# Performance work log

Measured on AMD Instinct MI355X. Metric: run time of the kernel, lower is better.

Reference implementation:

```python
import jax, jax.numpy as jnp
import numpy as np

N, E, T = 32768, 262144, 262144
DN, DE = 128, 128
EPS = 1e-5  # torch LayerNorm default eps


def layer_norm(x, g, b):
    m = jnp.mean(x, axis=-1, keepdims=True)
    v = jnp.mean((x - m) ** 2, axis=-1, keepdims=True)
    return (x - m) * jax.lax.rsqrt(v + EPS) * g + b


def setup_inputs() -> dict:
    key = jax.random.key(0)
    ks = jax.random.split(key, 16)
    node_embedding = jax.random.normal(ks[0], (N, DN), dtype=jnp.float32)
    edge_embedding = jax.random.normal(ks[1], (E, DE), dtype=jnp.float32)
    i = jax.random.randint(ks[2], (E,), 0, N)
    j = jax.random.randint(ks[3], (E,), 0, N)
    index_i = jax.random.randint(ks[4], (T,), 0, N)
    index_j = jax.random.randint(ks[5], (T,), 0, N)
    index_k = jax.random.randint(ks[6], (T,), 0, N)
    index_ji = jax.random.randint(ks[7], (T,), 0, E)
    index_kj = jax.random.randint(ks[8], (T,), 0, E)
    d3 = 3 * DN + 2 * DE
    W2 = jax.random.normal(ks[9], (2 * DE, DN), dtype=jnp.float32) / np.sqrt(DN)
    b2 = jnp.zeros((2 * DE,), dtype=jnp.float32)
    W3 = jax.random.normal(ks[10], (2 * DE, d3), dtype=jnp.float32) / np.sqrt(d3)
    b3 = jnp.zeros((2 * DE,), dtype=jnp.float32)
    g_c2 = jnp.ones((2 * DE,), jnp.float32); be_c2 = jnp.zeros((2 * DE,), jnp.float32)
    g_c3 = jnp.ones((2 * DE,), jnp.float32); be_c3 = jnp.zeros((2 * DE,), jnp.float32)
    g_c2_2 = jnp.ones((DE,), jnp.float32); be_c2_2 = jnp.zeros((DE,), jnp.float32)
    g_c3_2 = jnp.ones((DE,), jnp.float32); be_c3_2 = jnp.zeros((DE,), jnp.float32)
    return dict(node_embedding=node_embedding, edge_embedding=edge_embedding,
                i=i, j=j, index_i=index_i, index_j=index_j, index_k=index_k,
                index_ji=index_ji, index_kj=index_kj,
                W2=W2, b2=b2, W3=W3, b3=b3,
                g_c2=g_c2, be_c2=be_c2, g_c3=g_c3, be_c3=be_c3,
                g_c2_2=g_c2_2, be_c2_2=be_c2_2, g_c3_2=g_c3_2, be_c3_2=be_c3_2)


def reference(node_embedding, edge_embedding, i, j, index_i, index_j, index_k,
              index_ji, index_kj, W2, b2, W3, b3,
              g_c2, be_c2, g_c3, be_c3, g_c2_2, be_c2_2, g_c3_2, be_c3_2):
    num_edges = edge_embedding.shape[0]
    # --- c2 branch: per-edge elementwise product of endpoint node embeddings ---
    c2 = node_embedding[i] * node_embedding[j]                      # [E, Dn]
    c2 = layer_norm(c2 @ W2.T + b2, g_c2, be_c2)                    # [E, 2De]
    c2_filter, c2_core = jnp.split(c2, 2, axis=1)
    c2_emb = layer_norm(jax.nn.sigmoid(c2_filter) * jnp.tanh(c2_core), g_c2_2, be_c2_2)
    # --- c3 branch: triplet gather -> linear -> LN -> gate -> scatter-sum ---
    c3 = jnp.concatenate([node_embedding[index_i], node_embedding[index_j],
                          node_embedding[index_k], edge_embedding[index_ji],
                          edge_embedding[index_kj]], axis=1)        # [T, 3Dn+2De]
    c3 = layer_norm(c3 @ W3.T + b3, g_c3, be_c3)                    # [T, 2De]
    c3_filter, c3_core = jnp.split(c3, 2, axis=1)
    msg = jax.nn.sigmoid(c3_filter) * jnp.tanh(c3_core)             # [T, De]
    c3_emb = jax.ops.segment_sum(msg, index_ji, num_segments=num_edges)  # [E, De]
    c3_emb = layer_norm(c3_emb, g_c3_2, be_c3_2)
    return jnp.tanh(edge_embedding + c2_emb + c3_emb)
```

## Files before the change

### kernel.cpp

```cpp
#include <hip/hip_runtime.h>

typedef _Float16 h16;
typedef _Float16 h16x8 __attribute__((ext_vector_type(8)));
typedef float    f32x4 __attribute__((ext_vector_type(4)));

static constexpr int NN  = 32768;
static constexpr int EE  = 262144;
static constexpr int TT  = 262144;
static constexpr int D   = 128;
static constexpr int K3  = 640;
static constexpr int LDA = 72;
#define EPS 1e-5f

__device__ __forceinline__ float fast_rcp(float x) { return __builtin_amdgcn_rcpf(x); }
__device__ __forceinline__ float fast_tanh(float x) {
    const float e = __expf(2.f * x);
    return 1.f - 2.f * fast_rcp(e + 1.f);
}
__device__ __forceinline__ float fast_sig(float x) {
    return fast_rcp(1.f + __expf(-x));
}

__global__ __launch_bounds__(256) void cvt_f32_f16(
    const float* __restrict__ src, h16* __restrict__ dst, int n8)
{
    const int i = blockIdx.x * 256 + threadIdx.x;
    if (i >= n8) return;
    const float4* s = reinterpret_cast<const float4*>(src);
    const float4 a = s[2 * i], b = s[2 * i + 1];
    h16x8 o;
    o[0] = (h16)a.x; o[1] = (h16)a.y; o[2] = (h16)a.z; o[3] = (h16)a.w;
    o[4] = (h16)b.x; o[5] = (h16)b.y; o[6] = (h16)b.z; o[7] = (h16)b.w;
    *reinterpret_cast<h16x8*>(dst + 8 * i) = o;
}

__global__ __launch_bounds__(256) void cvt_edge_zero(
    const float* __restrict__ src, h16* __restrict__ dst,
    float* __restrict__ zbuf, int n8)
{
    const int i = blockIdx.x * 256 + threadIdx.x;
    if (i >= n8) return;
    const float4* s = reinterpret_cast<const float4*>(src);
    const float4 a = s[2 * i], b = s[2 * i + 1];
    h16x8 o;
    o[0] = (h16)a.x; o[1] = (h16)a.y; o[2] = (h16)a.z; o[3] = (h16)a.w;
    o[4] = (h16)b.x; o[5] = (h16)b.y; o[6] = (h16)b.z; o[7] = (h16)b.w;
    *reinterpret_cast<h16x8*>(dst + 8 * i) = o;
    const float4 z = {0.f, 0.f, 0.f, 0.f};
    float4* zp = reinterpret_cast<float4*>(zbuf);
    zp[2 * i]     = z;
    zp[2 * i + 1] = z;
}

__global__ __launch_bounds__(256) void cvt_w_t(
    const float* __restrict__ src, h16* __restrict__ dst, int K, int n8)
{
    const int t = blockIdx.x * 256 + threadIdx.x;
    if (t >= n8) return;
    const int d   = t * 8;
    const int c   = d >> 14;
    const int rem = d & 16383;
    const int q   = rem >> 11;
    const int n   = (rem >> 3) & 255;
    const int k   = c * 64 + q * 8;
    const float4* s = reinterpret_cast<const float4*>(src + (size_t)n * K + k);
    const float4 a = s[0], b = s[1];
    h16x8 o;
    o[0] = (h16)a.x; o[1] = (h16)a.y; o[2] = (h16)a.z; o[3] = (h16)a.w;
    o[4] = (h16)b.x; o[5] = (h16)b.y; o[6] = (h16)b.z; o[7] = (h16)b.w;
    *reinterpret_cast<h16x8*>(dst + d) = o;
}

__global__ __launch_bounds__(256, 2) void c3_kernel(
    const h16*  __restrict__ nodeh, const float* __restrict__ edge,
    const h16*  __restrict__ edgeh,
    const int* __restrict__ idx_i, const int* __restrict__ idx_j,
    const int* __restrict__ idx_k, const int* __restrict__ idx_ji,
    const int* __restrict__ idx_kj,
    const h16* __restrict__ W3t, const float* __restrict__ b3,
    const float* __restrict__ g3, const float* __restrict__ be3,
    float* __restrict__ acc3)
{
    __shared__ h16 As[128 * LDA];
    __shared__ h16 Bs[256 * LDA];

    const int tid  = threadIdx.x;
    const int lane = tid & 63;
    const int wave = tid >> 6;
    const int l15  = lane & 15;
    const int quad = lane >> 4;
    const int m0   = blockIdx.x * 128;

    f32x4 acc[2][16];
    #pragma unroll
    for (int mt = 0; mt < 2; ++mt)
        #pragma unroll
        for (int nt = 0; nt < 16; ++nt)
            acc[mt][nt] = (f32x4){0.f, 0.f, 0.f, 0.f};

    const int r8  = tid >> 3;
    const int sub = tid & 7;

    int rIdx[5][4];
    {
        const int* arrs[5] = {idx_i, idx_j, idx_k, idx_ji, idx_kj};
        #pragma unroll
        for (int sg = 0; sg < 5; ++sg)
            #pragma unroll
            for (int p = 0; p < 4; ++p)
                rIdx[sg][p] = arrs[sg][m0 + p * 32 + r8];
    }

    h16x8 av[4], bv[8];

#define LDC3(c)                                                                          \
    {                                                                                    \
        const int seg  = (c) >> 1;                                                       \
        const int half = (c) & 1;                                                        \
        _Pragma("unroll")                                                                \
        for (int p = 0; p < 4; ++p) {                                                    \
            const size_t row = (size_t)rIdx[seg][p];                                     \
            if (seg < 3) {                                                               \
                av[p] = *reinterpret_cast<const h16x8*>(                                 \
                    nodeh + row * D + half * 64 + sub * 8);                              \
            } else if (edgeh) {                                                          \
                av[p] = *reinterpret_cast<const h16x8*>(                                 \
                    edgeh + row * D + half * 64 + sub * 8);                              \
            } else {                                                                     \
                const float4* fp = reinterpret_cast<const float4*>(                      \
                    edge + row * D + half * 64 + sub * 8);                               \
                const float4 u = fp[0], vv = fp[1];                                      \
                h16x8 t;                                                                 \
                t[0] = (h16)u.x;  t[1] = (h16)u.y;  t[2] = (h16)u.z;  t[3] = (h16)u.w;   \
                t[4] = (h16)vv.x; t[5] = (h16)vv.y; t[6] = (h16)vv.z; t[7] = (h16)vv.w;  \
                av[p] = t;                                                               \
            }                                                                            \
        }                                                                                \
        const h16x8* wp = reinterpret_cast<const h16x8*>(W3t) + (c) * 2048 + tid;        \
        _Pragma("unroll")                                                                \
        for (int q = 0; q < 8; ++q) bv[q] = wp[q * 256];                                 \
    }

    LDC3(0);

    #pragma unroll 1
    for (int c = 0; c < 10; ++c) {
        __syncthreads();
        #pragma unroll
        for (int p = 0; p < 4; ++p)
            *reinterpret_cast<h16x8*>(&As[(p * 32 + r8) * LDA + sub * 8]) = av[p];
        h16x8* bd = reinterpret_cast<h16x8*>(&Bs[tid * LDA]);
        #pragma unroll
        for (int q = 0; q < 8; ++q) bd[q] = bv[q];
        __syncthreads();

        if (c < 9) LDC3(c + 1);

        #pragma unroll
        for (int kk = 0; kk < 64; kk += 32) {
            h16x8 a0 = *reinterpret_cast<const h16x8*>(&As[(wave*32      + l15) * LDA + kk + quad*8]);
            h16x8 a1 = *reinterpret_cast<const h16x8*>(&As[(wave*32 + 16 + l15) * LDA + kk + quad*8]);
            #pragma unroll
            for (int nt = 0; nt < 16; ++nt) {
                h16x8 b = *reinterpret_cast<const h16x8*>(&Bs[(nt*16 + l15) * LDA + kk + quad*8]);
                acc[0][nt] = __builtin_amdgcn_mfma_f32_16x16x32_f16(a0, b, acc[0][nt], 0, 0, 0);
                acc[1][nt] = __builtin_amdgcn_mfma_f32_16x16x32_f16(a1, b, acc[1][nt], 0, 0, 0);
            }
        }
    }
#undef LDC3

    float bias[16], gg[16], bb[16];
    #pragma unroll
    for (int nt = 0; nt < 16; ++nt) {
        const int cc = nt * 16 + l15;
        bias[nt] = b3[cc]; gg[nt] = g3[cc]; bb[nt] = be3[cc];
    }
    #pragma unroll
    for (int mt = 0; mt < 2; ++mt) {
        #pragma unroll
        for (int rg = 0; rg < 4; ++rg) {
            float v[16];
            float s = 0.f, s2 = 0.f;
            #pragma unroll
            for (int nt = 0; nt < 16; ++nt) {
                v[nt] = acc[mt][nt][rg] + bias[nt];
                s += v[nt]; s2 += v[nt] * v[nt];
            }
            #pragma unroll
            for (int m = 1; m < 16; m <<= 1) {
                s  += __shfl_xor(s,  m, 64);
                s2 += __shfl_xor(s2, m, 64);
            }
            const float mean = s * (1.f / 256.f);
            const float var  = s2 * (1.f / 256.f) - mean * mean;
            const float inv  = rsqrtf(var + EPS);
            const int rowg   = m0 + wave * 32 + mt * 16 + quad * 4 + rg;
            const size_t e   = (size_t)idx_ji[rowg];
            #pragma unroll
            for (int nt = 0; nt < 8; ++nt) {
                const float f   = (v[nt]     - mean) * inv * gg[nt]     + bb[nt];
                const float co  = (v[nt + 8] - mean) * inv * gg[nt + 8] + bb[nt + 8];
                const float msg = fast_sig(f) * fast_tanh(co);
                atomicAdd(&acc3[e * D + nt * 16 + l15], msg);
            }
        }
    }
}

__global__ __launch_bounds__(256, 2) void c2_kernel(
    const h16* __restrict__ nodeh,
    const int* __restrict__ ei, const int* __restrict__ ej,
    const h16* __restrict__ W2t, const float* __restrict__ b2,
    const float* __restrict__ g2, const float* __restrict__ be2,
    const float* __restrict__ g22, const float* __restrict__ be22,
    const float* __restrict__ g32, const float* __restrict__ be32,
    const float* __restrict__ edge,
    float* __restrict__ out)
{
    __shared__ h16 As[128 * LDA];
    __shared__ h16 Bs[256 * LDA];

    const int tid  = threadIdx.x;
    const int lane = tid & 63;
    const int wave = tid >> 6;
    const int l15  = lane & 15;
    const int quad = lane >> 4;
    const int m0   = blockIdx.x * 128;

    f32x4 acc[2][16];
    #pragma unroll
    for (int mt = 0; mt < 2; ++mt)
        #pragma unroll
        for (int nt = 0; nt < 16; ++nt)
            acc[mt][nt] = (f32x4){0.f, 0.f, 0.f, 0.f};

    const int r8  = tid >> 3;
    const int sub = tid & 7;

    int rI[4], rJ[4];
    #pragma unroll
    for (int p = 0; p < 4; ++p) {
        rI[p] = ei[m0 + p * 32 + r8];
        rJ[p] = ej[m0 + p * 32 + r8];
    }

    h16x8 av[4], bv[8];

#define LDC2(c)                                                                          \
    {                                                                                    \
        _Pragma("unroll")                                                                \
        for (int p = 0; p < 4; ++p) {                                                    \
            const h16x8 si = *reinterpret_cast<const h16x8*>(                            \
                nodeh + (size_t)rI[p] * D + (c) * 64 + sub * 8);                         \
            const h16x8 sj = *reinterpret_cast<const h16x8*>(                            \
                nodeh + (size_t)rJ[p] * D + (c) * 64 + sub * 8);                         \
            av[p] = si * sj;                                                             \
        }                                                                                \
        const h16x8* wp = reinterpret_cast<const h16x8*>(W2t) + (c) * 2048 + tid;        \
        _Pragma("unroll")                                                                \
        for (int q = 0; q < 8; ++q) bv[q] = wp[q * 256];                                 \
    }

    LDC2(0);

    #pragma unroll 1
    for (int c = 0; c < 2; ++c) {
        __syncthreads();
        #pragma unroll
        for (int p = 0; p < 4; ++p)
            *reinterpret_cast<h16x8*>(&As[(p * 32 + r8) * LDA + sub * 8]) = av[p];
        h16x8* bd = reinterpret_cast<h16x8*>(&Bs[tid * LDA]);
        #pragma unroll
        for (int q = 0; q < 8; ++q) bd[q] = bv[q];
        __syncthreads();

        if (c < 1) LDC2(c + 1);

        #pragma unroll
        for (int kk = 0; kk < 64; kk += 32) {
            h16x8 a0 = *reinterpret_cast<const h16x8*>(&As[(wave*32      + l15) * LDA + kk + quad*8]);
            h16x8 a1 = *reinterpret_cast<const h16x8*>(&As[(wave*32 + 16 + l15) * LDA + kk + quad*8]);
            #pragma unroll
            for (int nt = 0; nt < 16; ++nt) {
                h16x8 b = *reinterpret_cast<const h16x8*>(&Bs[(nt*16 + l15) * LDA + kk + quad*8]);
                acc[0][nt] = __builtin_amdgcn_mfma_f32_16x16x32_f16(a0, b, acc[0][nt], 0, 0, 0);
                acc[1][nt] = __builtin_amdgcn_mfma_f32_16x16x32_f16(a1, b, acc[1][nt], 0, 0, 0);
            }
        }
    }
#undef LDC2

    float bias[16], gg[16], bb[16];
    #pragma unroll
    for (int nt = 0; nt < 16; ++nt) {
        const int cc = nt * 16 + l15;
        bias[nt] = b2[cc]; gg[nt] = g2[cc]; bb[nt] = be2[cc];
    }
    float g2c[8], b2c[8], g3c[8], b3c[8];
    #pragma unroll
    for (int nt = 0; nt < 8; ++nt) {
        const int cc = nt * 16 + l15;
        g2c[nt] = g22[cc]; b2c[nt] = be22[cc];
        g3c[nt] = g32[cc]; b3c[nt] = be32[cc];
    }
    #pragma unroll
    for (int mt = 0; mt < 2; ++mt) {
        #pragma unroll
        for (int rg = 0; rg < 4; ++rg) {
            float v[16];
            float s = 0.f, s2 = 0.f;
            #pragma unroll
            for (int nt = 0; nt < 16; ++nt) {
                v[nt] = acc[mt][nt][rg] + bias[nt];
                s += v[nt]; s2 += v[nt] * v[nt];
            }
            #pragma unroll
            for (int m = 1; m < 16; m <<= 1) {
                s  += __shfl_xor(s,  m, 64);
                s2 += __shfl_xor(s2, m, 64);
            }
            const float mean = s * (1.f / 256.f);
            const float var  = s2 * (1.f / 256.f) - mean * mean;
            const float inv  = rsqrtf(var + EPS);
            const size_t rowg = (size_t)(m0 + wave * 32 + mt * 16 + quad * 4 + rg);

            float msg[8], a3[8];
            float t = 0.f, t2 = 0.f, u = 0.f, u2 = 0.f;
            #pragma unroll
            for (int nt = 0; nt < 8; ++nt) {
                const float f  = (v[nt]     - mean) * inv * gg[nt]     + bb[nt];
                const float co = (v[nt + 8] - mean) * inv * gg[nt + 8] + bb[nt + 8];
                const float m_ = fast_sig(f) * fast_tanh(co);
                msg[nt] = m_; t += m_; t2 += m_ * m_;
                const float a_ = out[rowg * D + nt * 16 + l15];
                a3[nt] = a_; u += a_; u2 += a_ * a_;
            }
            #pragma unroll
            for (int m = 1; m < 16; m <<= 1) {
                t  += __shfl_xor(t,  m, 64);
                t2 += __shfl_xor(t2, m, 64);
                u  += __shfl_xor(u,  m, 64);
                u2 += __shfl_xor(u2, m, 64);
            }
            const float mean2 = t * (1.f / 128.f);
            const float var2  = t2 * (1.f / 128.f) - mean2 * mean2;
            const float inv2  = rsqrtf(var2 + EPS);
            const float mean3 = u * (1.f / 128.f);
            const float var3  = u2 * (1.f / 128.f) - mean3 * mean3;
            const float inv3  = rsqrtf(var3 + EPS);
            #pragma unroll
            for (int nt = 0; nt < 8; ++nt) {
                const int cc = nt * 16 + l15;
                const float c2v = (msg[nt] - mean2) * inv2 * g2c[nt] + b2c[nt];
                const float c3v = (a3[nt]  - mean3) * inv3 * g3c[nt] + b3c[nt];
                const float ev  = edge[rowg * D + cc];
                out[rowg * D + cc] = fast_tanh(ev + c2v + c3v);
            }
        }
    }
}

extern "C" void kernel_launch(void* const* d_in, const int* in_sizes, int n_in,
                              void* d_out, int out_size, void* d_ws, size_t ws_size,
                              hipStream_t stream)
{
    const float* node   = (const float*)d_in[0];
    const float* edge   = (const float*)d_in[1];
    const int*   e_i    = (const int*)d_in[2];
    const int*   e_j    = (const int*)d_in[3];
    const int*   idx_i  = (const int*)d_in[4];
    const int*   idx_j  = (const int*)d_in[5];
    const int*   idx_k  = (const int*)d_in[6];
    const int*   idx_ji = (const int*)d_in[7];
    const int*   idx_kj = (const int*)d_in[8];
    const float* W2     = (const float*)d_in[9];
    const float* b2     = (const float*)d_in[10];
    const float* W3     = (const float*)d_in[11];
    const float* b3     = (const float*)d_in[12];
    const float* g_c2   = (const float*)d_in[13];
    const float* be_c2  = (const float*)d_in[14];
    const float* g_c3   = (const float*)d_in[15];
    const float* be_c3  = (const float*)d_in[16];
    const float* g_c22  = (const float*)d_in[17];
    const float* be_c22 = (const float*)d_in[18];
    const float* g_c32  = (const float*)d_in[19];
    const float* be_c32 = (const float*)d_in[20];

    h16* W3t   = (h16*)d_ws;
    h16* W2t   = W3t + 256 * K3;
    h16* nodeh = W2t + 256 * D;
    h16* edgeh = nodeh + (size_t)NN * D;
    const size_t need = ((size_t)256 * K3 + 256 * D + (size_t)NN * D
                         + (size_t)EE * D) * sizeof(h16);
    const bool use_edgeh = ws_size >= need;

    float* acc3 = (float*)d_out;
    float* out  = (float*)d_out;

    cvt_w_t<<<dim3((256 * K3 / 8 + 255) / 256), dim3(256), 0, stream>>>(W3, W3t, K3, 256 * K3 / 8);
    cvt_w_t<<<dim3((256 * D  / 8 + 255) / 256), dim3(256), 0, stream>>>(W2, W2t, D, 256 * D / 8);
    cvt_f32_f16<<<dim3((NN * D   / 8 + 255) / 256), dim3(256), 0, stream>>>(node, nodeh, NN * D / 8);
    if (use_edgeh) {
        cvt_edge_zero<<<dim3((EE * D / 8 + 255) / 256), dim3(256), 0, stream>>>(
            edge, edgeh, acc3, EE * D / 8);
    } else {
        hipMemsetAsync(d_out, 0, (size_t)EE * D * sizeof(float), stream);
    }

    c3_kernel<<<dim3(TT / 128), dim3(256), 0, stream>>>(
        nodeh, edge, use_edgeh ? edgeh : (const h16*)nullptr,
        idx_i, idx_j, idx_k, idx_ji, idx_kj, W3t, b3, g_c3, be_c3, acc3);
    c2_kernel<<<dim3(EE / 128), dim3(256), 0, stream>>>(
        nodeh, e_i, e_j, W2t, b2, g_c2, be_c2, g_c22, be_c22,
        g_c32, be_c32, edge, out);
}
```

Before: 614.7 us.

## Gather A operands directly into MFMA registers and pre-swizzle weights to fragment order

The A tile is no longer staged through LDS. Each lane gathers its own gathered-row fragments straight into registers in MFMA operand layout, and loads for the next chunk are double-buffered in registers. The weight conversion kernel now writes W in per-lane fragment order, so B reads from LDS become contiguous, conflict-free vector loads and the padded LDA layout is dropped. This cuts LDS traffic and shared memory footprint, but gathers are now per-lane 16-byte loads with less coalescing, and the extra prefetch buffers raise register pressure.

```diff
diff --git a/kernel.cpp b/kernel.cpp
--- a/kernel.cpp
+++ b/kernel.cpp
@@ -9,7 +9,6 @@
 static constexpr int TT  = 262144;
 static constexpr int D   = 128;
 static constexpr int K3  = 640;
-static constexpr int LDA = 72;
 #define EPS 1e-5f
 
 __device__ __forceinline__ float fast_rcp(float x) { return __builtin_amdgcn_rcpf(x); }
@@ -52,19 +51,21 @@
     zp[2 * i + 1] = z;
 }
 
-__global__ __launch_bounds__(256) void cvt_w_t(
+__global__ __launch_bounds__(256) void cvt_w_fo(
     const float* __restrict__ src, h16* __restrict__ dst, int K, int n8)
 {
     const int t = blockIdx.x * 256 + threadIdx.x;
     if (t >= n8) return;
-    const int d   = t * 8;
-    const int c   = d >> 14;
-    const int rem = d & 16383;
-    const int q   = rem >> 11;
-    const int n   = (rem >> 3) & 255;
-    const int k   = c * 64 + q * 8;
-    const float4* s = reinterpret_cast<const float4*>(src + (size_t)n * K + k);
-    const float4 a = s[0], b = s[1];
+    const int d    = t * 8;
+    const int c    = d >> 14;
+    const int s    = (d >> 3) & 2047;
+    const int tile = s >> 6;
+    const int ln   = s & 63;
+    const int quad = ln >> 4, l15 = ln & 15;
+    const int n    = (tile >> 1) * 16 + l15;
+    const int k    = c * 64 + (tile & 1) * 32 + quad * 8;
+    const float4* sp = reinterpret_cast<const float4*>(src + (size_t)n * K + k);
+    const float4 a = sp[0], b = sp[1];
     h16x8 o;
     o[0] = (h16)a.x; o[1] = (h16)a.y; o[2] = (h16)a.z; o[3] = (h16)a.w;
     o[4] = (h16)b.x; o[5] = (h16)b.y; o[6] = (h16)b.z; o[7] = (h16)b.w;
@@ -81,8 +82,8 @@
     const float* __restrict__ g3, const float* __restrict__ be3,
     float* __restrict__ acc3)
 {
-    __shared__ h16 As[128 * LDA];
-    __shared__ h16 Bs[256 * LDA];
+    __shared__ h16 Bs[256 * 64];
+    h16x8* Bsv = reinterpret_cast<h16x8*>(Bs);
 
     const int tid  = threadIdx.x;
     const int lane = tid & 63;
@@ -98,77 +99,94 @@
         for (int nt = 0; nt < 16; ++nt)
             acc[mt][nt] = (f32x4){0.f, 0.f, 0.f, 0.f};
 
-    const int r8  = tid >> 3;
-    const int sub = tid & 7;
-
-    int rIdx[5][4];
-    {
-        const int* arrs[5] = {idx_i, idx_j, idx_k, idx_ji, idx_kj};
-        #pragma unroll
-        for (int sg = 0; sg < 5; ++sg)
-            #pragma unroll
-            for (int p = 0; p < 4; ++p)
-                rIdx[sg][p] = arrs[sg][m0 + p * 32 + r8];
-    }
-
-    h16x8 av[4], bv[8];
-
-#define LDC3(c)                                                                          \
+    const int row0 = m0 + wave * 32 + l15;
+    const int rI0  = idx_i [row0],      rI1  = idx_i [row0 + 16];
+    const int rJ0  = idx_j [row0],      rJ1  = idx_j [row0 + 16];
+    const int rK0  = idx_k [row0],      rK1  = idx_k [row0 + 16];
+    const int rJI0 = idx_ji[row0],      rJI1 = idx_ji[row0 + 16];
+    const int rKJ0 = idx_kj[row0],      rKJ1 = idx_kj[row0 + 16];
+
+    h16x8 cur[4], nxt[4], bv[8];
+
+#define LDA3(c, dstv)                                                                    \
     {                                                                                    \
         const int seg  = (c) >> 1;                                                       \
         const int half = (c) & 1;                                                        \
-        _Pragma("unroll")                                                                \
-        for (int p = 0; p < 4; ++p) {                                                    \
-            const size_t row = (size_t)rIdx[seg][p];                                     \
-            if (seg < 3) {                                                               \
-                av[p] = *reinterpret_cast<const h16x8*>(                                 \
-                    nodeh + row * D + half * 64 + sub * 8);                              \
-            } else if (edgeh) {                                                          \
-                av[p] = *reinterpret_cast<const h16x8*>(                                 \
-                    edgeh + row * D + half * 64 + sub * 8);                              \
-            } else {                                                                     \
-                const float4* fp = reinterpret_cast<const float4*>(                      \
-                    edge + row * D + half * 64 + sub * 8);                               \
-                const float4 u = fp[0], vv = fp[1];                                      \
-                h16x8 t;                                                                 \
-                t[0] = (h16)u.x;  t[1] = (h16)u.y;  t[2] = (h16)u.z;  t[3] = (h16)u.w;   \
-                t[4] = (h16)vv.x; t[5] = (h16)vv.y; t[6] = (h16)vv.z; t[7] = (h16)vv.w;  \
-                av[p] = t;                                                               \
+        const size_t R0 = (size_t)((seg == 0) ? rI0 : (seg == 1) ? rJ0                   \
+                         : (seg == 2) ? rK0 : (seg == 3) ? rJI0 : rKJ0);                 \
+        const size_t R1 = (size_t)((seg == 0) ? rI1 : (seg == 1) ? rJ1                   \
+                         : (seg == 2) ? rK1 : (seg == 3) ? rJI1 : rKJ1);                 \
+        if (seg < 3) {                                                                   \
+            _Pragma("unroll")                                                            \
+            for (int kki = 0; kki < 2; ++kki) {                                          \
+                dstv[kki]     = *reinterpret_cast<const h16x8*>(                         \
+                    nodeh + R0 * D + half * 64 + kki * 32 + quad * 8);                   \
+                dstv[2 + kki] = *reinterpret_cast<const h16x8*>(                         \
+                    nodeh + R1 * D + half * 64 + kki * 32 + quad * 8);                   \
+            }                                                                            \
+        } else if (edgeh) {                                                              \
+            _Pragma("unroll")                                                            \
+            for (int kki = 0; kki < 2; ++kki) {                                          \
+                dstv[kki]     = *reinterpret_cast<const h16x8*>(                         \
+                    edgeh + R0 * D + half * 64 + kki * 32 + quad * 8);                   \
+                dstv[2 + kki] = *reinterpret_cast<const h16x8*>(                         \
+                    edgeh + R1 * D + half * 64 + kki * 32 + quad * 8);                   \
+            }                                                                            \
+        } else {                                                                         \
+            _Pragma("unroll")                                                            \
+            for (int kki = 0; kki < 2; ++kki) {                                          \
+                _Pragma("unroll")                                                        \
+                for (int m2 = 0; m2 < 2; ++m2) {                                         \
+                    const size_t RR = m2 ? R1 : R0;                                      \
+                    const float4* fp = reinterpret_cast<const float4*>(                  \
+                        edge + RR * D + half * 64 + kki * 32 + quad * 8);                \
+                    const float4 u = fp[0], vv = fp[1];                                  \
+                    h16x8 t;                                                             \
+                    t[0] = (h16)u.x;  t[1] = (h16)u.y;  t[2] = (h16)u.z;  t[3] = (h16)u.w;\
+                    t[4] = (h16)vv.x; t[5] = (h16)vv.y; t[6] = (h16)vv.z; t[7] = (h16)vv.w;\
+                    dstv[2 * m2 + kki] = t;                                              \
+                }                                                                        \
             }                                                                            \
         }                                                                                \
-        const h16x8* wp = reinterpret_cast<const h16x8*>(W3t) + (c) * 2048 + tid;        \
+    }
+
+#define LDB3(c)                                                                          \
+    {                                                                                    \
+        const h16x8* wp = reinterpret_cast<const h16x8*>(W3t) + (size_t)(c) * 2048 + tid;\
         _Pragma("unroll")                                                                \
         for (int q = 0; q < 8; ++q) bv[q] = wp[q * 256];                                 \
     }
 
-    LDC3(0);
+    LDA3(0, cur);
+    LDB3(0);
 
     #pragma unroll 1
     for (int c = 0; c < 10; ++c) {
         __syncthreads();
         #pragma unroll
-        for (int p = 0; p < 4; ++p)
-            *reinterpret_cast<h16x8*>(&As[(p * 32 + r8) * LDA + sub * 8]) = av[p];
-        h16x8* bd = reinterpret_cast<h16x8*>(&Bs[tid * LDA]);
-        #pragma unroll
-        for (int q = 0; q < 8; ++q) bd[q] = bv[q];
+        for (int q = 0; q < 8; ++q) Bsv[q * 256 + tid] = bv[q];
         __syncthreads();
 
-        if (c < 9) LDC3(c + 1);
-
-        #pragma unroll
-        for (int kk = 0; kk < 64; kk += 32) {
-            h16x8 a0 = *reinterpret_cast<const h16x8*>(&As[(wave*32      + l15) * LDA + kk + quad*8]);
-            h16x8 a1 = *reinterpret_cast<const h16x8*>(&As[(wave*32 + 16 + l15) * LDA + kk + quad*8]);
+        if (c < 9) { LDB3(c + 1); LDA3(c + 1, nxt); }
+
+        #pragma unroll
+        for (int kki = 0; kki < 2; ++kki) {
+            const h16x8 a0 = cur[kki];
+            const h16x8 a1 = cur[2 + kki];
             #pragma unroll
             for (int nt = 0; nt < 16; ++nt) {
-                h16x8 b = *reinterpret_cast<const h16x8*>(&Bs[(nt*16 + l15) * LDA + kk + quad*8]);
+                const h16x8 b = Bsv[(nt * 2 + kki) * 64 + lane];
                 acc[0][nt] = __builtin_amdgcn_mfma_f32_16x16x32_f16(a0, b, acc[0][nt], 0, 0, 0);
                 acc[1][nt] = __builtin_amdgcn_mfma_f32_16x16x32_f16(a1, b, acc[1][nt], 0, 0, 0);
             }
         }
-    }
-#undef LDC3
+        if (c < 9) {
+            #pragma unroll
+            for (int q = 0; q < 4; ++q) cur[q] = nxt[q];
+        }
+    }
+#undef LDA3
+#undef LDB3
 
     float bias[16], gg[16], bb[16];
     #pragma unroll
@@ -218,8 +236,8 @@
     const float* __restrict__ edge,
     float* __restrict__ out)
 {
-    __shared__ h16 As[128 * LDA];
-    __shared__ h16 Bs[256 * LDA];
+    __shared__ h16 Bs[256 * 64];
+    h16x8* Bsv = reinterpret_cast<h16x8*>(Bs);
 
     const int tid  = threadIdx.x;
     const int lane = tid & 63;
@@ -235,61 +253,63 @@
         for (int nt = 0; nt < 16; ++nt)
             acc[mt][nt] = (f32x4){0.f, 0.f, 0.f, 0.f};
 
-    const int r8  = tid >> 3;
-    const int sub = tid & 7;
-
-    int rI[4], rJ[4];
-    #pragma unroll
-    for (int p = 0; p < 4; ++p) {
-        rI[p] = ei[m0 + p * 32 + r8];
-        rJ[p] = ej[m0 + p * 32 + r8];
-    }
-
-    h16x8 av[4], bv[8];
-
-#define LDC2(c)                                                                          \
+    const int row0 = m0 + wave * 32 + l15;
+    const size_t rI0 = (size_t)ei[row0], rI1 = (size_t)ei[row0 + 16];
+    const size_t rJ0 = (size_t)ej[row0], rJ1 = (size_t)ej[row0 + 16];
+
+    h16x8 cur[4], nxt[4], bv[8];
+
+#define LDA2(c, dstv)                                                                    \
     {                                                                                    \
         _Pragma("unroll")                                                                \
-        for (int p = 0; p < 4; ++p) {                                                    \
-            const h16x8 si = *reinterpret_cast<const h16x8*>(                            \
-                nodeh + (size_t)rI[p] * D + (c) * 64 + sub * 8);                         \
-            const h16x8 sj = *reinterpret_cast<const h16x8*>(                            \
-                nodeh + (size_t)rJ[p] * D + (c) * 64 + sub * 8);                         \
-            av[p] = si * sj;                                                             \
+        for (int kki = 0; kki < 2; ++kki) {                                              \
+            const int off = (c) * 64 + kki * 32 + quad * 8;                              \
+            const h16x8 si0 = *reinterpret_cast<const h16x8*>(nodeh + rI0 * D + off);    \
+            const h16x8 sj0 = *reinterpret_cast<const h16x8*>(nodeh + rJ0 * D + off);    \
+            const h16x8 si1 = *reinterpret_cast<const h16x8*>(nodeh + rI1 * D + off);    \
+            const h16x8 sj1 = *reinterpret_cast<const h16x8*>(nodeh + rJ1 * D + off);    \
+            dstv[kki]     = si0 * sj0;                                                   \
+            dstv[2 + kki] = si1 * sj1;                                                   \
         }                                                                                \
-        const h16x8* wp = reinterpret_cast<const h16x8*>(W2t) + (c) * 2048 + tid;        \
+    }
+
+#define LDB2(c)                                                                          \
+    {                                                                                    \
+        const h16x8* wp = reinterpret_cast<const h16x8*>(W2t) + (size_t)(c) * 2048 + tid;\
         _Pragma("unroll")                                                                \
         for (int q = 0; q < 8; ++q) bv[q] = wp[q * 256];                                 \
     }
 
-    LDC2(0);
+    LDA2(0, cur);
+    LDB2(0);
 
     #pragma unroll 1
     for (int c = 0; c < 2; ++c) {
         __syncthreads();
         #pragma unroll
-        for (int p = 0; p < 4; ++p)
-            *reinterpret_cast<h16x8*>(&As[(p * 32 + r8) * LDA + sub * 8]) = av[p];
-        h16x8* bd = reinterpret_cast<h16x8*>(&Bs[tid * LDA]);
-        #pragma unroll
-        for (int q = 0; q < 8; ++q) bd[q] = bv[q];
+        for (int q = 0; q < 8; ++q) Bsv[q * 256 + tid] = bv[q];
         __syncthreads();
 
-        if (c < 1) LDC2(c + 1);
-
-        #pragma unroll
-        for (int kk = 0; kk < 64; kk += 32) {
-            h16x8 a0 = *reinterpret_cast<const h16x8*>(&As[(wave*32      + l15) * LDA + kk + quad*8]);
-            h16x8 a1 = *reinterpret_cast<const h16x8*>(&As[(wave*32 + 16 + l15) * LDA + kk + quad*8]);
+        if (c < 1) { LDB2(c + 1); LDA2(c + 1, nxt); }
+
+        #pragma unroll
+        for (int kki = 0; kki < 2; ++kki) {
+            const h16x8 a0 = cur[kki];
+            const h16x8 a1 = cur[2 + kki];
             #pragma unroll
             for (int nt = 0; nt < 16; ++nt) {
-                h16x8 b = *reinterpret_cast<const h16x8*>(&Bs[(nt*16 + l15) * LDA + kk + quad*8]);
+                const h16x8 b = Bsv[(nt * 2 + kki) * 64 + lane];
                 acc[0][nt] = __builtin_amdgcn_mfma_f32_16x16x32_f16(a0, b, acc[0][nt], 0, 0, 0);
                 acc[1][nt] = __builtin_amdgcn_mfma_f32_16x16x32_f16(a1, b, acc[1][nt], 0, 0, 0);
             }
         }
-    }
-#undef LDC2
+        if (c < 1) {
+            #pragma unroll
+            for (int q = 0; q < 4; ++q) cur[q] = nxt[q];
+        }
+    }
+#undef LDA2
+#undef LDB2
 
     float bias[16], gg[16], bb[16];
     #pragma unroll
@@ -398,8 +418,8 @@
     float* acc3 = (float*)d_out;
     float* out  = (float*)d_out;
 
-    cvt_w_t<<<dim3((256 * K3 / 8 + 255) / 256), dim3(256), 0, stream>>>(W3, W3t, K3, 256 * K3 / 8);
-    cvt_w_t<<<dim3((256 * D  / 8 + 255) / 256), dim3(256), 0, stream>>>(W2, W2t, D, 256 * D / 8);
+    cvt_w_fo<<<dim3((256 * K3 / 8 + 255) / 256), dim3(256), 0, stream>>>(W3, W3t, K3, 256 * K3 / 8);
+    cvt_w_fo<<<dim3((256 * D  / 8 + 255) / 256), dim3(256), 0, stream>>>(W2, W2t, D, 256 * D / 8);
     cvt_f32_f16<<<dim3((NN * D   / 8 + 255) / 256), dim3(256), 0, stream>>>(node, nodeh, NN * D / 8);
     if (use_edgeh) {
         cvt_edge_zero<<<dim3((EE * D / 8 + 255) / 256), dim3(256), 0, stream>>>(
```

Measured after the change: 603.4 us. No clear change (-1.8%).
